# Optimization experiments

Measured on AMD Instinct MI355X. Metric: run time of the kernel, lower is better.

The kernel has to match this reference:

```python
import jax, jax.numpy as jnp
import numpy as np

ALPHA = 0.2
BETA = 1.0
TEMPERATURE = 0.05
EPS = 1e-8  # torch cosine_similarity eps


def setup_inputs() -> dict:
    key = jax.random.key(0)
    k1, k2 = jax.random.split(key)
    B, R, D = 4096, 18, 256  # rows, segment size (1 anchor + 1 pos + 16 negs), embed dim
    features = jax.random.normal(k1, (B * R, D), dtype=jnp.float32)
    scores = jax.random.normal(k2, (B * (R - 1),), dtype=jnp.float32)
    row_sizes = jnp.full((B,), R, dtype=jnp.int32)  # uniform ragged sizes
    logit_scale = jnp.array([1.0 / TEMPERATURE], dtype=jnp.float32)
    return {"features": features, "scores": scores, "row_sizes": row_sizes,
            "logit_scale": logit_scale}


def reference(features, scores, row_sizes, logit_scale):
    B = row_sizes.shape[0]
    R = features.shape[0] // B  # uniform segment size
    D = features.shape[1]
    f3 = features.reshape(B, R, D)
    anchor = f3[:, 0]          # [B, D]
    tgt = f3[:, 1:]            # [B, R-1, D]  (positive first, then negatives)

    # --- per-row cosine sims + log_softmax + KLDiv(batchmean) ---
    an = jnp.maximum(jnp.linalg.norm(anchor, axis=-1, keepdims=True), EPS)  # [B,1]
    tn = jnp.maximum(jnp.linalg.norm(tgt, axis=-1), EPS)                    # [B,R-1]
    cos = jnp.einsum('bd,bkd->bk', anchor, tgt) / (an * tn)                 # [B,R-1]
    emb_log = jax.nn.log_softmax(cos, axis=-1)                              # [B,R-1]
    ce = jax.nn.softmax(scores.reshape(B, R - 1), axis=-1)                  # [B,R-1]
    # torch KLDivLoss(reduction='batchmean') on a length-(R-1) vector divides by (R-1)
    kl = jnp.sum(ce * (jnp.log(ce) - emb_log), axis=-1) / (R - 1)           # [B]
    loss = jnp.mean(BETA * kl)

    # --- single InfoNCE over all rows: anchors vs [positives; all negatives] ---
    pos = f3[:, 1]                                   # [B, D]
    negs = f3[:, 2:].reshape(B * (R - 2), D)         # [B*(R-2), D]
    targets = jnp.concatenate([pos, negs], axis=0)   # [B*(R-1), D]
    logits = logit_scale[0] * (anchor @ targets.T)   # [B, B*(R-1)]
    labels = jnp.arange(B)
    # cross_entropy(logits, labels) with mean reduction
    infonce = jnp.mean(jax.nn.logsumexp(logits, axis=-1) - logits[labels, labels])

    return loss + ALPHA * infonce
```

## Files before the change

### kernel.cpp

```cpp
#include <hip/hip_runtime.h>
#include <math.h>

#define ALPHA 0.2f
#define BETA 1.0f
#define EPSV 1e-8f
#define LOG2E 1.4426950408889634f
#define LN2 0.6931471805599453f

#define BATCH 4096
#define RR 18
#define KT 17
#define DD 256
#define NTGT (BATCH*KT)
#define NTILE (NTGT/32)
#define TILE_BYTES (32*DD)

#define AG 64
#define NSPLIT 32
#define TPS (NTILE/NSPLIT)

#define EXPA 8388608.0f
#define EXPB 1064880320.0f

typedef int   i32x8  __attribute__((ext_vector_type(8)));
typedef float f32x16 __attribute__((ext_vector_type(16)));

__device__ inline int pk8(float a, float b, float c, float d){
  int p = __builtin_amdgcn_cvt_pk_fp8_f32(a, b, 0, false);
  return  __builtin_amdgcn_cvt_pk_fp8_f32(c, d, p, true);
}

__device__ inline float fmax3(float a, float b, float c){
  return fmaxf(fmaxf(a, b), c);
}

__device__ inline float fexp2u(float x, float kc){
  float t = fmaf(x, EXPA, kc);
  unsigned u;
  asm("v_cvt_u32_f32 %0, %1" : "=v"(u) : "v"(t));
  return __uint_as_float(u);
}


__global__ __launch_bounds__(256) void prep_kernel(
    const float* __restrict__ feat, const float* __restrict__ scores,
    const float* __restrict__ lscale,
    unsigned char* __restrict__ abf8, unsigned char* __restrict__ tbf8,
    float* __restrict__ diag, float* __restrict__ klarr,
    float* __restrict__ out){
  __shared__ float csh[KT];
  int b = blockIdx.x, tid = threadIdx.x;
  int grp = tid >> 4, j = tid & 15;
  const float* fb = feat + (size_t)b * RR * DD;
  float s2 = lscale[0] * LOG2E;

  if (b == 0 && tid == 0) out[0] = 0.f;

  float4 a0 = ((const float4*)fb)[j*4+0];
  float4 a1 = ((const float4*)fb)[j*4+1];
  float4 a2 = ((const float4*)fb)[j*4+2];
  float4 a3 = ((const float4*)fb)[j*4+3];
  float asq = (a0.x*a0.x+a0.y*a0.y+a0.z*a0.z+a0.w*a0.w)
            + (a1.x*a1.x+a1.y*a1.y+a1.z*a1.z+a1.w*a1.w)
            + (a2.x*a2.x+a2.y*a2.y+a2.z*a2.z+a2.w*a2.w)
            + (a3.x*a3.x+a3.y*a3.y+a3.z*a3.z+a3.w*a3.w);
  #pragma unroll
  for (int off=1; off<16; off<<=1) asq += __shfl_xor(asq, off);
  float an = fmaxf(sqrtf(asq), EPSV);

  if (tid < 16){
    uint4 v = make_uint4(
      (unsigned)pk8(a0.x*s2,a0.y*s2,a0.z*s2,a0.w*s2),
      (unsigned)pk8(a1.x*s2,a1.y*s2,a1.z*s2,a1.w*s2),
      (unsigned)pk8(a2.x*s2,a2.y*s2,a2.z*s2,a2.w*s2),
      (unsigned)pk8(a3.x*s2,a3.y*s2,a3.z*s2,a3.w*s2));
    *(uint4*)(abf8 + (size_t)b*DD + j*16) = v;
  }

  for (int kr = grp+1; kr <= KT; kr += 16){
    const float4* tp = (const float4*)(fb + (size_t)kr*DD) + j*4;
    float4 t0=tp[0], t1=tp[1], t2=tp[2], t3=tp[3];
    int t  = b*KT + (kr-1);
    int tile = t >> 5, m = t & 31;
    int ki = j >> 2, hf = (j >> 1) & 1, w = j & 1;
    uint4 v = make_uint4(
      (unsigned)pk8(t0.x,t0.y,t0.z,t0.w), (unsigned)pk8(t1.x,t1.y,t1.z,t1.w),
      (unsigned)pk8(t2.x,t2.y,t2.z,t2.w), (unsigned)pk8(t3.x,t3.y,t3.z,t3.w));
    *(uint4*)(tbf8 + (size_t)tile*TILE_BYTES + ki*2048 + w*1024 + hf*512 + m*16) = v;
    float d = (a0.x*t0.x+a0.y*t0.y+a0.z*t0.z+a0.w*t0.w)
            + (a1.x*t1.x+a1.y*t1.y+a1.z*t1.z+a1.w*t1.w)
            + (a2.x*t2.x+a2.y*t2.y+a2.z*t2.z+a2.w*t2.w)
            + (a3.x*t3.x+a3.y*t3.y+a3.z*t3.z+a3.w*t3.w);
    float q = (t0.x*t0.x+t0.y*t0.y+t0.z*t0.z+t0.w*t0.w)
            + (t1.x*t1.x+t1.y*t1.y+t1.z*t1.z+t1.w*t1.w)
            + (t2.x*t2.x+t2.y*t2.y+t2.z*t2.z+t2.w*t2.w)
            + (t3.x*t3.x+t3.y*t3.y+t3.z*t3.z+t3.w*t3.w);
    #pragma unroll
    for (int off=1; off<16; off<<=1){ d += __shfl_xor(d,off); q += __shfl_xor(q,off); }
    if (j == 0){
      csh[kr-1] = d / (an * fmaxf(sqrtf(q), EPSV));
      if (kr == 1) diag[b] = d;
    }
  }
  __syncthreads();

  if (tid < 64){
    bool act = tid < KT;
    float c  = act ? csh[tid] : -INFINITY;
    float sv = act ? scores[(size_t)b*KT + tid] : -INFINITY;
    float cm = c, sm = sv;
    #pragma unroll
    for (int off=1; off<64; off<<=1){
      cm = fmaxf(cm, __shfl_xor(cm, off));
      sm = fmaxf(sm, __shfl_xor(sm, off));
    }
    float ec = act ? __builtin_amdgcn_exp2f((c -cm)*LOG2E) : 0.f;
    float es = act ? __builtin_amdgcn_exp2f((sv-sm)*LOG2E) : 0.f;
    float cs = ec, ss = es;
    #pragma unroll
    for (int off=1; off<64; off<<=1){
      cs += __shfl_xor(cs, off);
      ss += __shfl_xor(ss, off);
    }
    float lse_c = cm + __logf(cs);
    float lse_s = sm + __logf(ss);
    float kt = 0.f;
    if (act){
      float lq = sv - lse_s;
      float lp = c  - lse_c;
      kt = __builtin_amdgcn_exp2f(lq*LOG2E)*(lq - lp);
    }
    #pragma unroll
    for (int off=1; off<64; off<<=1) kt += __shfl_xor(kt, off);
    if (tid == 0) klarr[b] = kt * (1.0f/KT);
  }
}

__global__ __launch_bounds__(64,2) void gemm_lse_kernel(
    const unsigned char* __restrict__ abf8, const unsigned char* __restrict__ tbf8,
    float* __restrict__ part_m, float* __restrict__ part_s){
  const int bid  = blockIdx.x;
  const int ns   = (bid & 7)*4 + ((bid >> 3) & 3);
  const int ag   = bid >> 5;
  const int lane = threadIdx.x;
  const int l31  = lane & 31;
  const int half = lane >> 5;

  i32x8 af[2][4];
  {
    const unsigned char* ab = abf8 + (size_t)ag*64*DD;
    #pragma unroll
    for (int nt=0;nt<2;++nt)
      #pragma unroll
      for (int ki=0;ki<4;++ki){
        const unsigned char* p = ab + (size_t)(nt*32+l31)*DD + ki*64 + half*32;
        uint4 lo = *(const uint4*)p;
        uint4 hi = *(const uint4*)(p+16);
        af[nt][ki] = (i32x8){(int)lo.x,(int)lo.y,(int)lo.z,(int)lo.w,
                             (int)hi.x,(int)hi.y,(int)hi.z,(int)hi.w};
      }
  }

  const unsigned char* gbase =
      tbf8 + (size_t)(ns*TPS)*TILE_BYTES + half*512 + l31*16;

  i32x8 ta[4], tb[4];
  auto ld = [&](int tt, i32x8 tf[4]){
    const unsigned char* p = gbase + (size_t)tt*TILE_BYTES;
    #pragma unroll
    for (int ki=0;ki<4;++ki){
      uint4 lo = *(const uint4*)(p + ki*2048);
      uint4 hi = *(const uint4*)(p + ki*2048 + 1024);
      tf[ki] = (i32x8){(int)lo.x,(int)lo.y,(int)lo.z,(int)lo.w,
                       (int)hi.x,(int)hi.y,(int)hi.z,(int)hi.w};
    }
  };

  float run_m[2] = {-INFINITY,-INFINITY};
  float run_s[2] = {0.f,0.f};
  f32x16 acc[2];

  auto mfma_tile = [&](i32x8 tf[4]){
    acc[0] = (f32x16)(0.f);
    acc[1] = (f32x16)(0.f);
    __builtin_amdgcn_s_setprio(1);
    #pragma unroll
    for (int ki=0;ki<4;++ki){
      acc[0] = __builtin_amdgcn_mfma_scale_f32_32x32x64_f8f6f4(
                   tf[ki], af[0][ki], acc[0], 0,0, 0,127, 0,127);
      acc[1] = __builtin_amdgcn_mfma_scale_f32_32x32x64_f8f6f4(
                   tf[ki], af[1][ki], acc[1], 0,0, 0,127, 0,127);
    }
    __builtin_amdgcn_s_setprio(0);
  };

  auto epilogue = [&](){
    #pragma unroll
    for (int nt=0;nt<2;++nt){
      f32x16 t = acc[nt];
      float x0 = fmax3(t[0], t[1], t[2]);
      float x1 = fmax3(t[3], t[4], t[5]);
      float x2 = fmax3(t[6], t[7], t[8]);
      float x3 = fmax3(t[9], t[10], t[11]);
      float x4 = fmax3(t[12], t[13], t[14]);
      float mx = fmaxf(fmax3(x0,x1,x2), fmax3(x3,x4,t[15]));

      float kc = fmaf(mx, -EXPA, EXPB);
      float s0=0.f, s1=0.f, s2=0.f, s3=0.f;
      #pragma unroll
      for (int r=0;r<16;r+=4){
        s0 += fexp2u(t[r  ],kc);
        s1 += fexp2u(t[r+1],kc);
        s2 += fexp2u(t[r+2],kc);
        s3 += fexp2u(t[r+3],kc);
      }
      float sh = (s0+s1)+(s2+s3);

      float nm = fmaxf(run_m[nt], mx);
      run_s[nt] = run_s[nt]*__builtin_amdgcn_exp2f(run_m[nt]-nm)
                + sh*__builtin_amdgcn_exp2f(mx-nm);
      run_m[nt] = nm;
    }
  };

  ld(0, ta);
  ld(1, tb);
  for (int t=0; t<TPS; t+=2){
    mfma_tile(ta);
    if (t+2 < TPS) ld(t+2, ta);
    epilogue();
    mfma_tile(tb);
    if (t+3 < TPS) ld(t+3, tb);
    epilogue();
  }

  #pragma unroll
  for (int nt=0;nt<2;++nt){
    float om = __shfl_xor(run_m[nt], 32);
    float os = __shfl_xor(run_s[nt], 32);
    float nm = fmaxf(run_m[nt], om);
    float S  = run_s[nt]*__builtin_amdgcn_exp2f(run_m[nt]-nm)
             + os*__builtin_amdgcn_exp2f(om-nm);
    if (half == 0){
      int gm = ag*64 + nt*32 + l31;
      part_m[(size_t)ns*BATCH + gm] = nm;
      part_s[(size_t)ns*BATCH + gm] = S;
    }
  }
}

__global__ __launch_bounds__(256) void combine_kernel(
    const float* __restrict__ part_m, const float* __restrict__ part_s,
    const float* __restrict__ diag, const float* __restrict__ klarr,
    const float* __restrict__ lscale, float* __restrict__ out){
  int tid = threadIdx.x;
  int b = blockIdx.x*256 + tid;
  float s = lscale[0];
  float m = -INFINITY, S = 0.f;
  #pragma unroll
  for (int ns=0; ns<NSPLIT; ++ns){
    float pm_ = part_m[(size_t)ns*BATCH + b];
    float ps_ = part_s[(size_t)ns*BATCH + b];
    float nm = fmaxf(m, pm_);
    S = S*__builtin_amdgcn_exp2f(m-nm) + ps_*__builtin_amdgcn_exp2f(pm_-nm);
    m = nm;
  }
  float inf = (m + __log2f(S))*LN2 - s*diag[b];
  float c = BETA*klarr[b] + ALPHA*inf;
  #pragma unroll
  for (int off=1; off<64; off<<=1) c += __shfl_xor(c, off);
  if ((tid & 63) == 0) atomicAdd(out, c*(1.0f/BATCH));
}

extern "C" void kernel_launch(void* const* d_in, const int* in_sizes, int n_in,
                              void* d_out, int out_size, void* d_ws, size_t ws_size,
                              hipStream_t stream){
  const float* feat   = (const float*)d_in[0];
  const float* scores = (const float*)d_in[1];
  const float* lscale = (const float*)d_in[3];

  float* ws     = (float*)d_ws;
  float* diag   = ws;
  float* klarr  = diag + BATCH;
  float* part_m = klarr + BATCH;
  float* part_s = part_m + (size_t)NSPLIT*BATCH;
  unsigned char* abf8 = (unsigned char*)(part_s + (size_t)NSPLIT*BATCH);
  unsigned char* tbf8 = abf8 + (size_t)BATCH*DD;

  float* outp = (float*)d_out;
  prep_kernel<<<BATCH, 256, 0, stream>>>(feat, scores, lscale, abf8, tbf8,
                                         diag, klarr, outp);
  gemm_lse_kernel<<<AG*NSPLIT, 64, 0, stream>>>(abf8, tbf8, part_m, part_s);
  combine_kernel<<<BATCH/256, 256, 0, stream>>>(part_m, part_s, diag, klarr,
                                                lscale, outp);
}
```

Baseline: 190.0 us.

## Stage fp8 target writes through LDS and pack epilogue math with packed-fp32 ops

The prep kernel now buffers the fp8-packed target rows in shared memory and writes them to the tiled global layout in a second pass, so the global stores are reorganized. The GEMM kernel loads fragments by writing halves of the vector registers directly, uses a zero-constant accumulator for the first MFMA instead of zeroing first, and computes the exp-approximation sums with v_pk_fma_f32/v_pk_add_f32. The online logsumexp update now needs only one exp2 per step instead of two, using a branch-free select. These are several unrelated micro-optimizations aimed at epilogue ALU cost and store coalescing; the inline asm may constrain register allocation and scheduling.

```diff
diff --git a/kernel.cpp b/kernel.cpp
--- a/kernel.cpp
+++ b/kernel.cpp
@@ -24,6 +24,7 @@
 
 typedef int   i32x8  __attribute__((ext_vector_type(8)));
 typedef float f32x16 __attribute__((ext_vector_type(16)));
+typedef float f32x2  __attribute__((ext_vector_type(2)));
 
 __device__ inline int pk8(float a, float b, float c, float d){
   int p = __builtin_amdgcn_cvt_pk_fp8_f32(a, b, 0, false);
@@ -34,10 +35,21 @@
   return fmaxf(fmaxf(a, b), c);
 }
 
-__device__ inline float fexp2u(float x, float kc){
-  float t = fmaf(x, EXPA, kc);
+__device__ inline f32x2 pk_fma2(f32x2 a, f32x2 b, f32x2 c){
+  f32x2 d;
+  asm("v_pk_fma_f32 %0, %1, %2, %3" : "=v"(d) : "v"(a), "v"(b), "v"(c));
+  return d;
+}
+
+__device__ inline f32x2 pk_add2(f32x2 a, f32x2 b){
+  f32x2 d;
+  asm("v_pk_add_f32 %0, %1, %2" : "=v"(d) : "v"(a), "v"(b));
+  return d;
+}
+
+__device__ inline float cvtbit(float x){
   unsigned u;
-  asm("v_cvt_u32_f32 %0, %1" : "=v"(u) : "v"(t));
+  asm("v_cvt_u32_f32 %0, %1" : "=v"(u) : "v"(x));
   return __uint_as_float(u);
 }
 
@@ -49,6 +61,7 @@
     float* __restrict__ diag, float* __restrict__ klarr,
     float* __restrict__ out){
   __shared__ float csh[KT];
+  __shared__ uint4 fsh[16][KT];
   int b = blockIdx.x, tid = threadIdx.x;
   int grp = tid >> 4, j = tid & 15;
   const float* fb = feat + (size_t)b * RR * DD;
@@ -80,13 +93,10 @@
   for (int kr = grp+1; kr <= KT; kr += 16){
     const float4* tp = (const float4*)(fb + (size_t)kr*DD) + j*4;
     float4 t0=tp[0], t1=tp[1], t2=tp[2], t3=tp[3];
-    int t  = b*KT + (kr-1);
-    int tile = t >> 5, m = t & 31;
-    int ki = j >> 2, hf = (j >> 1) & 1, w = j & 1;
     uint4 v = make_uint4(
       (unsigned)pk8(t0.x,t0.y,t0.z,t0.w), (unsigned)pk8(t1.x,t1.y,t1.z,t1.w),
       (unsigned)pk8(t2.x,t2.y,t2.z,t2.w), (unsigned)pk8(t3.x,t3.y,t3.z,t3.w));
-    *(uint4*)(tbf8 + (size_t)tile*TILE_BYTES + ki*2048 + w*1024 + hf*512 + m*16) = v;
+    fsh[j][kr-1] = v;
     float d = (a0.x*t0.x+a0.y*t0.y+a0.z*t0.z+a0.w*t0.w)
             + (a1.x*t1.x+a1.y*t1.y+a1.z*t1.z+a1.w*t1.w)
             + (a2.x*t2.x+a2.y*t2.y+a2.z*t2.z+a2.w*t2.w)
@@ -103,6 +113,15 @@
     }
   }
   __syncthreads();
+
+  for (int idx = tid; idx < 16*KT; idx += 256){
+    int jj = idx / KT, r = idx % KT;
+    uint4 v = fsh[jj][r];
+    int t = b*KT + r;
+    int tile = t >> 5, m = t & 31;
+    int ki = jj >> 2, hf = (jj >> 1) & 1, w = jj & 1;
+    *(uint4*)(tbf8 + (size_t)tile*TILE_BYTES + ki*2048 + w*1024 + hf*512 + m*16) = v;
+  }
 
   if (tid < 64){
     bool act = tid < KT;
@@ -154,10 +173,9 @@
       #pragma unroll
       for (int ki=0;ki<4;++ki){
         const unsigned char* p = ab + (size_t)(nt*32+l31)*DD + ki*64 + half*32;
-        uint4 lo = *(const uint4*)p;
-        uint4 hi = *(const uint4*)(p+16);
-        af[nt][ki] = (i32x8){(int)lo.x,(int)lo.y,(int)lo.z,(int)lo.w,
-                             (int)hi.x,(int)hi.y,(int)hi.z,(int)hi.w};
+        uint4* h = (uint4*)&af[nt][ki];
+        h[0] = *(const uint4*)p;
+        h[1] = *(const uint4*)(p+16);
       }
   }
 
@@ -169,23 +187,26 @@
     const unsigned char* p = gbase + (size_t)tt*TILE_BYTES;
     #pragma unroll
     for (int ki=0;ki<4;++ki){
-      uint4 lo = *(const uint4*)(p + ki*2048);
-      uint4 hi = *(const uint4*)(p + ki*2048 + 1024);
-      tf[ki] = (i32x8){(int)lo.x,(int)lo.y,(int)lo.z,(int)lo.w,
-                       (int)hi.x,(int)hi.y,(int)hi.z,(int)hi.w};
+      uint4* h = (uint4*)&tf[ki];
+      h[0] = *(const uint4*)(p + ki*2048);
+      h[1] = *(const uint4*)(p + ki*2048 + 1024);
     }
   };
 
   float run_m[2] = {-INFINITY,-INFINITY};
   float run_s[2] = {0.f,0.f};
   f32x16 acc[2];
+  const f32x16 vzero = (f32x16)(0.f);
+  f32x2 A2; A2[0]=EXPA; A2[1]=EXPA;
 
   auto mfma_tile = [&](i32x8 tf[4]){
-    acc[0] = (f32x16)(0.f);
-    acc[1] = (f32x16)(0.f);
     __builtin_amdgcn_s_setprio(1);
-    #pragma unroll
-    for (int ki=0;ki<4;++ki){
+    acc[0] = __builtin_amdgcn_mfma_scale_f32_32x32x64_f8f6f4(
+                 tf[0], af[0][0], vzero, 0,0, 0,127, 0,127);
+    acc[1] = __builtin_amdgcn_mfma_scale_f32_32x32x64_f8f6f4(
+                 tf[0], af[1][0], vzero, 0,0, 0,127, 0,127);
+    #pragma unroll
+    for (int ki=1;ki<4;++ki){
       acc[0] = __builtin_amdgcn_mfma_scale_f32_32x32x64_f8f6f4(
                    tf[ki], af[0][ki], acc[0], 0,0, 0,127, 0,127);
       acc[1] = __builtin_amdgcn_mfma_scale_f32_32x32x64_f8f6f4(
@@ -206,20 +227,28 @@
       float mx = fmaxf(fmax3(x0,x1,x2), fmax3(x3,x4,t[15]));
 
       float kc = fmaf(mx, -EXPA, EXPB);
-      float s0=0.f, s1=0.f, s2=0.f, s3=0.f;
+      f32x2 kc2; kc2[0]=kc; kc2[1]=kc;
+      f32x2 s01; s01[0]=0.f; s01[1]=0.f;
+      f32x2 s23; s23[0]=0.f; s23[1]=0.f;
       #pragma unroll
       for (int r=0;r<16;r+=4){
-        s0 += fexp2u(t[r  ],kc);
-        s1 += fexp2u(t[r+1],kc);
-        s2 += fexp2u(t[r+2],kc);
-        s3 += fexp2u(t[r+3],kc);
+        f32x2 p0; p0[0]=t[r];   p0[1]=t[r+1];
+        f32x2 p1; p1[0]=t[r+2]; p1[1]=t[r+3];
+        f32x2 e0 = pk_fma2(p0, A2, kc2);
+        f32x2 e1 = pk_fma2(p1, A2, kc2);
+        f32x2 u0; u0[0]=cvtbit(e0[0]); u0[1]=cvtbit(e0[1]);
+        f32x2 u1; u1[0]=cvtbit(e1[0]); u1[1]=cvtbit(e1[1]);
+        s01 = pk_add2(s01, u0);
+        s23 = pk_add2(s23, u1);
       }
-      float sh = (s0+s1)+(s2+s3);
-
-      float nm = fmaxf(run_m[nt], mx);
-      run_s[nt] = run_s[nt]*__builtin_amdgcn_exp2f(run_m[nt]-nm)
-                + sh*__builtin_amdgcn_exp2f(mx-nm);
-      run_m[nt] = nm;
+      f32x2 sp = pk_add2(s01, s23);
+      float sh = sp[0] + sp[1];
+
+      float d = mx - run_m[nt];
+      float e = __builtin_amdgcn_exp2f(-fabsf(d));
+      bool g  = d > 0.f;
+      run_s[nt] = g ? fmaf(run_s[nt], e, sh) : fmaf(sh, e, run_s[nt]);
+      run_m[nt] = g ? mx : run_m[nt];
     }
   };
 
```

After: 194.4 us. 1.02x slower.

## Double split count, stage fp8 tiles through LDS, init MFMA from zero

Applied to the files above, without the earlier changes.

Doubles the number of target splits in the GEMM+logsumexp kernel, so each block handles fewer tiles and more blocks run across the GPU. In the prep kernel, the scattered fp8 tile stores now go to shared memory first and are written out in a second loop, aiming for better-coalesced global writes. The first MFMA now takes a constant zero accumulator instead of explicitly zeroing acc, and fragment loads write straight into vector halves. More splits also means more partial results for the final reduction to combine.

```diff
diff --git a/kernel.cpp b/kernel.cpp
--- a/kernel.cpp
+++ b/kernel.cpp
@@ -16,7 +16,7 @@
 #define TILE_BYTES (32*DD)
 
 #define AG 64
-#define NSPLIT 32
+#define NSPLIT 64
 #define TPS (NTILE/NSPLIT)
 
 #define EXPA 8388608.0f
@@ -49,6 +49,7 @@
     float* __restrict__ diag, float* __restrict__ klarr,
     float* __restrict__ out){
   __shared__ float csh[KT];
+  __shared__ uint4 fsh[16][KT];
   int b = blockIdx.x, tid = threadIdx.x;
   int grp = tid >> 4, j = tid & 15;
   const float* fb = feat + (size_t)b * RR * DD;
@@ -80,13 +81,10 @@
   for (int kr = grp+1; kr <= KT; kr += 16){
     const float4* tp = (const float4*)(fb + (size_t)kr*DD) + j*4;
     float4 t0=tp[0], t1=tp[1], t2=tp[2], t3=tp[3];
-    int t  = b*KT + (kr-1);
-    int tile = t >> 5, m = t & 31;
-    int ki = j >> 2, hf = (j >> 1) & 1, w = j & 1;
     uint4 v = make_uint4(
       (unsigned)pk8(t0.x,t0.y,t0.z,t0.w), (unsigned)pk8(t1.x,t1.y,t1.z,t1.w),
       (unsigned)pk8(t2.x,t2.y,t2.z,t2.w), (unsigned)pk8(t3.x,t3.y,t3.z,t3.w));
-    *(uint4*)(tbf8 + (size_t)tile*TILE_BYTES + ki*2048 + w*1024 + hf*512 + m*16) = v;
+    fsh[j][kr-1] = v;
     float d = (a0.x*t0.x+a0.y*t0.y+a0.z*t0.z+a0.w*t0.w)
             + (a1.x*t1.x+a1.y*t1.y+a1.z*t1.z+a1.w*t1.w)
             + (a2.x*t2.x+a2.y*t2.y+a2.z*t2.z+a2.w*t2.w)
@@ -104,6 +102,15 @@
   }
   __syncthreads();
 
+  for (int idx = tid; idx < 16*KT; idx += 256){
+    int jj = idx / KT, r = idx % KT;
+    uint4 v = fsh[jj][r];
+    int t = b*KT + r;
+    int tile = t >> 5, m = t & 31;
+    int ki = jj >> 2, hf = (jj >> 1) & 1, w = jj & 1;
+    *(uint4*)(tbf8 + (size_t)tile*TILE_BYTES + ki*2048 + w*1024 + hf*512 + m*16) = v;
+  }
+
   if (tid < 64){
     bool act = tid < KT;
     float c  = act ? csh[tid] : -INFINITY;
@@ -140,8 +147,8 @@
     const unsigned char* __restrict__ abf8, const unsigned char* __restrict__ tbf8,
     float* __restrict__ part_m, float* __restrict__ part_s){
   const int bid  = blockIdx.x;
-  const int ns   = (bid & 7)*4 + ((bid >> 3) & 3);
-  const int ag   = bid >> 5;
+  const int ns   = (bid & 7)*8 + ((bid >> 3) & 7);
+  const int ag   = bid >> 6;
   const int lane = threadIdx.x;
   const int l31  = lane & 31;
   const int half = lane >> 5;
@@ -154,10 +161,9 @@
       #pragma unroll
       for (int ki=0;ki<4;++ki){
         const unsigned char* p = ab + (size_t)(nt*32+l31)*DD + ki*64 + half*32;
-        uint4 lo = *(const uint4*)p;
-        uint4 hi = *(const uint4*)(p+16);
-        af[nt][ki] = (i32x8){(int)lo.x,(int)lo.y,(int)lo.z,(int)lo.w,
-                             (int)hi.x,(int)hi.y,(int)hi.z,(int)hi.w};
+        uint4* h = (uint4*)&af[nt][ki];
+        h[0] = *(const uint4*)p;
+        h[1] = *(const uint4*)(p+16);
       }
   }
 
@@ -169,23 +175,25 @@
     const unsigned char* p = gbase + (size_t)tt*TILE_BYTES;
     #pragma unroll
     for (int ki=0;ki<4;++ki){
-      uint4 lo = *(const uint4*)(p + ki*2048);
-      uint4 hi = *(const uint4*)(p + ki*2048 + 1024);
-      tf[ki] = (i32x8){(int)lo.x,(int)lo.y,(int)lo.z,(int)lo.w,
-                       (int)hi.x,(int)hi.y,(int)hi.z,(int)hi.w};
+      uint4* h = (uint4*)&tf[ki];
+      h[0] = *(const uint4*)(p + ki*2048);
+      h[1] = *(const uint4*)(p + ki*2048 + 1024);
     }
   };
 
   float run_m[2] = {-INFINITY,-INFINITY};
   float run_s[2] = {0.f,0.f};
   f32x16 acc[2];
+  const f32x16 vzero = (f32x16)(0.f);
 
   auto mfma_tile = [&](i32x8 tf[4]){
-    acc[0] = (f32x16)(0.f);
-    acc[1] = (f32x16)(0.f);
     __builtin_amdgcn_s_setprio(1);
-    #pragma unroll
-    for (int ki=0;ki<4;++ki){
+    acc[0] = __builtin_amdgcn_mfma_scale_f32_32x32x64_f8f6f4(
+                 tf[0], af[0][0], vzero, 0,0, 0,127, 0,127);
+    acc[1] = __builtin_amdgcn_mfma_scale_f32_32x32x64_f8f6f4(
+                 tf[0], af[1][0], vzero, 0,0, 0,127, 0,127);
+    #pragma unroll
+    for (int ki=1;ki<4;++ki){
       acc[0] = __builtin_amdgcn_mfma_scale_f32_32x32x64_f8f6f4(
                    tf[ki], af[0][ki], acc[0], 0,0, 0,127, 0,127);
       acc[1] = __builtin_amdgcn_mfma_scale_f32_32x32x64_f8f6f4(
```

Result: slower. 194.8 us (+2.5%).
